# Performance work log

Hardware: AMD Instinct MI355X
Metric: run time of the kernel (lower is better)

The kernel has to match this reference:

```python
import jax, jax.numpy as jnp
import numpy as np

B = 1024       # batch_size b (features has 2*b rows)
DIM = 128      # feature dim
EPS = 1.0      # euclidean eps (module default)


def _make_neighbor_indices(b):
    # negative_samples (2048) >= 2*b - 1 -> deterministic full-batch branch
    idx = np.arange(b)
    not_self = ~np.eye(b, dtype=bool)
    neg1 = np.broadcast_to(idx[None, :], (b, b))[not_self].reshape(b, b - 1)
    neg2 = neg1 + b  # arange(b, 2b) excluding self position
    pos = (idx + b)[:, None]  # positive pair index, column 0
    return np.concatenate([pos, neg1, neg2], axis=1)  # [b, 2b-1]


def setup_inputs() -> dict:
    key = jax.random.key(0)
    features = jax.random.normal(key, (2 * B, DIM), dtype=jnp.float32)
    neigh_inds = jnp.asarray(_make_neighbor_indices(B), dtype=jnp.int64)
    return {"features": features, "neigh_inds": neigh_inds}


def reference(features, neigh_inds):
    b = features.shape[0] // 2
    neighbors = features[neigh_inds]            # [b, 2b-1, d] gather
    origs = features[:b]                        # [b, d]
    # squared euclidean distances anchor -> each neighbor
    dists = jnp.sum((origs[:, None, :] - neighbors) ** 2, axis=2)  # [b, 2b-1]
    probits = 1.0 / (EPS + dists)               # Cauchy kernel
    # infonce: positive is column 0 (clamp is (-inf, inf) -> identity)
    loss = -(jnp.log(probits[:, 0]) - jnp.log(jnp.sum(probits, axis=1)))
    return jnp.mean(loss)
```

## Files before the change

### kernel.cpp

```cpp
#include <hip/hip_runtime.h>
#include <hip/hip_bf16.h>

static constexpr int kB   = 1024;
static constexpr int kNF  = 2048;
static constexpr int kDIM = 128;

typedef __attribute__((ext_vector_type(8))) short  short8;
typedef __attribute__((ext_vector_type(4))) float  floatx4;

__global__ __launch_bounds__(256) void k_prep(const float* __restrict__ F,
                                              __hip_bfloat162* __restrict__ Fb2,
                                              float* __restrict__ norms,
                                              float* __restrict__ S,
                                              float* __restrict__ out) {
    const int t    = threadIdx.x;
    const int lane = t & 63;
    const int row  = blockIdx.x * 4 + (t >> 6);

    const float2 v = *(const float2*)(F + row * kDIM + lane * 2);

    __hip_bfloat162 bv;
    bv.x = __float2bfloat16(v.x);
    bv.y = __float2bfloat16(v.y);
    Fb2[row * (kDIM / 2) + lane] = bv;

    float n = v.x * v.x + v.y * v.y;
    #pragma unroll
    for (int off = 1; off < 64; off <<= 1) n += __shfl_xor(n, off, 64);
    if (lane == 0) norms[row] = n;

    if (blockIdx.x < 4) S[blockIdx.x * 256 + t] = 0.0f;
    if (blockIdx.x == 4 && t == 0) out[0] = 0.0f;
}

static constexpr int kLdsRow = kDIM + 8;

__global__ __launch_bounds__(256) void k_main(const unsigned short* __restrict__ Fb,
                                              const float* __restrict__ norms,
                                              float* __restrict__ S,
                                              float* __restrict__ P) {
    __shared__ unsigned short As[64 * kLdsRow];
    __shared__ unsigned short Bs[64 * kLdsRow];

    const int t  = threadIdx.x;
    const int i0 = blockIdx.x * 64;
    const int k0 = blockIdx.y * 64;

    #pragma unroll
    for (int e = 0; e < 4; ++e) {
        const int idx = e * 256 + t;
        const int row = idx >> 4;
        const int c   = idx & 15;
        const uint4 va = *(const uint4*)(Fb + (i0 + row) * kDIM + c * 8);
        const uint4 vb = *(const uint4*)(Fb + (k0 + row) * kDIM + c * 8);
        *(uint4*)(As + row * kLdsRow + c * 8) = va;
        *(uint4*)(Bs + row * kLdsRow + c * 8) = vb;
    }
    __syncthreads();

    const int lane = t & 63;
    const int w    = t >> 6;
    const int q    = lane >> 4;
    const int c    = lane & 15;

    floatx4 acc[4] = {{0.f,0.f,0.f,0.f},{0.f,0.f,0.f,0.f},
                      {0.f,0.f,0.f,0.f},{0.f,0.f,0.f,0.f}};

    const int arow = w * 16 + c;
    #pragma unroll
    for (int ks = 0; ks < 4; ++ks) {
        const short8 a = *(const short8*)(As + arow * kLdsRow + ks * 32 + q * 8);
        #pragma unroll
        for (int nt = 0; nt < 4; ++nt) {
            const short8 b = *(const short8*)(Bs + (nt * 16 + c) * kLdsRow + ks * 32 + q * 8);
            acc[nt] = __builtin_amdgcn_mfma_f32_16x16x32_bf16(a, b, acc[nt], 0, 0, 0);
        }
    }

    const int ibase = i0 + w * 16 + q * 4;
    float ni[4];
    #pragma unroll
    for (int r = 0; r < 4; ++r) ni[r] = norms[ibase + r];

    float psum[4] = {0.f, 0.f, 0.f, 0.f};
    #pragma unroll
    for (int nt = 0; nt < 4; ++nt) {
        const int   kg = k0 + nt * 16 + c;
        const float nk = norms[kg];
        #pragma unroll
        for (int r = 0; r < 4; ++r) {
            const int ig = ibase + r;
            float dist = ni[r] + nk - 2.0f * acc[nt][r];
            float p    = 1.0f / (1.0f + dist);
            if (kg == ig) p = 0.0f;
            psum[r] += p;
            if (kg == ig + kB) P[ig] = p;
        }
    }

    #pragma unroll
    for (int off = 1; off < 16; off <<= 1) {
        #pragma unroll
        for (int r = 0; r < 4; ++r) psum[r] += __shfl_xor(psum[r], off, 64);
    }
    if (c == 0) {
        #pragma unroll
        for (int r = 0; r < 4; ++r) atomicAdd(&S[ibase + r], psum[r]);
    }
}

__global__ __launch_bounds__(256) void k_final(const float* __restrict__ S,
                                               const float* __restrict__ P,
                                               float* __restrict__ out) {
    const int i = blockIdx.x * 256 + threadIdx.x;
    float l = __logf(S[i]) - __logf(P[i]);
    #pragma unroll
    for (int off = 1; off < 64; off <<= 1) l += __shfl_xor(l, off, 64);
    if ((threadIdx.x & 63) == 0) atomicAdd(out, l * (1.0f / (float)kB));
}

extern "C" void kernel_launch(void* const* d_in, const int* in_sizes, int n_in,
                              void* d_out, int out_size, void* d_ws, size_t ws_size,
                              hipStream_t stream) {
    const float* F = (const float*)d_in[0];
    float* out = (float*)d_out;

    char* ws = (char*)d_ws;
    unsigned short* Fb    = (unsigned short*)ws;
    float*          norms = (float*)(ws + 524288);
    float*          S     = (float*)(ws + 524288 + 8192);
    float*          P     = (float*)(ws + 524288 + 8192 + 4096);

    k_prep <<<dim3(512),    dim3(256), 0, stream>>>(F, (__hip_bfloat162*)Fb, norms, S, out);
    k_main <<<dim3(16, 32), dim3(256), 0, stream>>>(Fb, norms, S, P);
    k_final<<<dim3(4),      dim3(256), 0, stream>>>(S, P, out);
}
```

Baseline: 68.10 us.

## Load MFMA operands directly from global and replace atomics with partial-sum reduction

The main kernel drops its LDS staging and barrier. Each wave now loads its bf16 A and B fragments straight from global memory into registers, with 8 waves per block splitting the 64x64 tile into 16x32 sub-tiles. The row-sum atomics are replaced by per-block partial sums written to a buffer. A single 1024-thread final kernel then reduces those partials and writes the mean, so the zero-initialisation in the prep kernel is no longer needed. This removes atomic contention and LDS traffic, at the cost of redundant global and L2 reads and a larger workspace.

```diff
diff --git a/kernel.cpp b/kernel.cpp
--- a/kernel.cpp
+++ b/kernel.cpp
@@ -1,18 +1,18 @@
 #include <hip/hip_runtime.h>
 #include <hip/hip_bf16.h>
 
+
 static constexpr int kB   = 1024;
-static constexpr int kNF  = 2048;
 static constexpr int kDIM = 128;
+static constexpr int kGX  = 16;
+static constexpr int kGY  = 32;
 
 typedef __attribute__((ext_vector_type(8))) short  short8;
 typedef __attribute__((ext_vector_type(4))) float  floatx4;
 
 __global__ __launch_bounds__(256) void k_prep(const float* __restrict__ F,
                                               __hip_bfloat162* __restrict__ Fb2,
-                                              float* __restrict__ norms,
-                                              float* __restrict__ S,
-                                              float* __restrict__ out) {
+                                              float* __restrict__ norms) {
     const int t    = threadIdx.x;
     const int lane = t & 63;
     const int row  = blockIdx.x * 4 + (t >> 6);
@@ -28,64 +28,55 @@
     #pragma unroll
     for (int off = 1; off < 64; off <<= 1) n += __shfl_xor(n, off, 64);
     if (lane == 0) norms[row] = n;
-
-    if (blockIdx.x < 4) S[blockIdx.x * 256 + t] = 0.0f;
-    if (blockIdx.x == 4 && t == 0) out[0] = 0.0f;
 }
 
-static constexpr int kLdsRow = kDIM + 8;
+__global__ __launch_bounds__(512) void k_main(const unsigned short* __restrict__ Fb,
+                                              const float* __restrict__ norms,
+                                              float* __restrict__ Spart,
+                                              float* __restrict__ P) {
+    __shared__ float sred[4][16][2];
 
-__global__ __launch_bounds__(256) void k_main(const unsigned short* __restrict__ Fb,
-                                              const float* __restrict__ norms,
-                                              float* __restrict__ S,
-                                              float* __restrict__ P) {
-    __shared__ unsigned short As[64 * kLdsRow];
-    __shared__ unsigned short Bs[64 * kLdsRow];
-
-    const int t  = threadIdx.x;
-    const int i0 = blockIdx.x * 64;
-    const int k0 = blockIdx.y * 64;
-
-    #pragma unroll
-    for (int e = 0; e < 4; ++e) {
-        const int idx = e * 256 + t;
-        const int row = idx >> 4;
-        const int c   = idx & 15;
-        const uint4 va = *(const uint4*)(Fb + (i0 + row) * kDIM + c * 8);
-        const uint4 vb = *(const uint4*)(Fb + (k0 + row) * kDIM + c * 8);
-        *(uint4*)(As + row * kLdsRow + c * 8) = va;
-        *(uint4*)(Bs + row * kLdsRow + c * 8) = vb;
-    }
-    __syncthreads();
-
+    const int t    = threadIdx.x;
+    const int w    = t >> 6;
+    const int wi   = w >> 1;
+    const int wk   = w & 1;
     const int lane = t & 63;
-    const int w    = t >> 6;
     const int q    = lane >> 4;
     const int c    = lane & 15;
+    const int i0   = blockIdx.x * 64;
+    const int k0   = blockIdx.y * 64;
 
-    floatx4 acc[4] = {{0.f,0.f,0.f,0.f},{0.f,0.f,0.f,0.f},
-                      {0.f,0.f,0.f,0.f},{0.f,0.f,0.f,0.f}};
+    const unsigned short* Arow = Fb + (i0 + wi * 16 + c) * kDIM;
+    short8 a[4];
+    #pragma unroll
+    for (int ks = 0; ks < 4; ++ks)
+        a[ks] = *(const short8*)(Arow + ks * 32 + q * 8);
 
-    const int arow = w * 16 + c;
+    short8 b[2][4];
+    #pragma unroll
+    for (int nt = 0; nt < 2; ++nt) {
+        const unsigned short* Brow = Fb + (k0 + wk * 32 + nt * 16 + c) * kDIM;
+        #pragma unroll
+        for (int ks = 0; ks < 4; ++ks)
+            b[nt][ks] = *(const short8*)(Brow + ks * 32 + q * 8);
+    }
+
+    floatx4 acc[2] = {{0.f,0.f,0.f,0.f},{0.f,0.f,0.f,0.f}};
     #pragma unroll
     for (int ks = 0; ks < 4; ++ks) {
-        const short8 a = *(const short8*)(As + arow * kLdsRow + ks * 32 + q * 8);
-        #pragma unroll
-        for (int nt = 0; nt < 4; ++nt) {
-            const short8 b = *(const short8*)(Bs + (nt * 16 + c) * kLdsRow + ks * 32 + q * 8);
-            acc[nt] = __builtin_amdgcn_mfma_f32_16x16x32_bf16(a, b, acc[nt], 0, 0, 0);
-        }
+        acc[0] = __builtin_amdgcn_mfma_f32_16x16x32_bf16(a[ks], b[0][ks], acc[0], 0, 0, 0);
+        acc[1] = __builtin_amdgcn_mfma_f32_16x16x32_bf16(a[ks], b[1][ks], acc[1], 0, 0, 0);
     }
 
-    const int ibase = i0 + w * 16 + q * 4;
+    const int ibase = i0 + wi * 16 + q * 4;
     float ni[4];
     #pragma unroll
     for (int r = 0; r < 4; ++r) ni[r] = norms[ibase + r];
 
     float psum[4] = {0.f, 0.f, 0.f, 0.f};
     #pragma unroll
-    for (int nt = 0; nt < 4; ++nt) {
-        const int   kg = k0 + nt * 16 + c;
+    for (int nt = 0; nt < 2; ++nt) {
+        const int   kg = k0 + wk * 32 + nt * 16 + c;
         const float nk = norms[kg];
         #pragma unroll
         for (int r = 0; r < 4; ++r) {
@@ -105,18 +96,37 @@
     }
     if (c == 0) {
         #pragma unroll
-        for (int r = 0; r < 4; ++r) atomicAdd(&S[ibase + r], psum[r]);
+        for (int r = 0; r < 4; ++r) sred[wi][q * 4 + r][wk] = psum[r];
+    }
+    __syncthreads();
+
+    if (t < 64) {
+        const float s = sred[t >> 4][t & 15][0] + sred[t >> 4][t & 15][1];
+        Spart[blockIdx.y * kB + i0 + t] = s;
     }
 }
 
-__global__ __launch_bounds__(256) void k_final(const float* __restrict__ S,
-                                               const float* __restrict__ P,
-                                               float* __restrict__ out) {
-    const int i = blockIdx.x * 256 + threadIdx.x;
-    float l = __logf(S[i]) - __logf(P[i]);
+__global__ __launch_bounds__(1024) void k_final(const float* __restrict__ Spart,
+                                                const float* __restrict__ P,
+                                                float* __restrict__ out) {
+    __shared__ float wred[16];
+    const int t = threadIdx.x;
+
+    float s = 0.f;
+    #pragma unroll
+    for (int kb = 0; kb < kGY; ++kb) s += Spart[kb * kB + t];
+
+    float l = __logf(s) - __logf(P[t]);
     #pragma unroll
     for (int off = 1; off < 64; off <<= 1) l += __shfl_xor(l, off, 64);
-    if ((threadIdx.x & 63) == 0) atomicAdd(out, l * (1.0f / (float)kB));
+    if ((t & 63) == 0) wred[t >> 6] = l;
+    __syncthreads();
+    if (t == 0) {
+        float tot = 0.f;
+        #pragma unroll
+        for (int j = 0; j < 16; ++j) tot += wred[j];
+        out[0] = tot * (1.0f / (float)kB);
+    }
 }
 
 extern "C" void kernel_launch(void* const* d_in, const int* in_sizes, int n_in,
@@ -128,10 +138,10 @@
     char* ws = (char*)d_ws;
     unsigned short* Fb    = (unsigned short*)ws;
     float*          norms = (float*)(ws + 524288);
-    float*          S     = (float*)(ws + 524288 + 8192);
-    float*          P     = (float*)(ws + 524288 + 8192 + 4096);
+    float*          Spart = (float*)(ws + 524288 + 8192);
+    float*          P     = (float*)(ws + 524288 + 8192 + 131072);
 
-    k_prep <<<dim3(512),    dim3(256), 0, stream>>>(F, (__hip_bfloat162*)Fb, norms, S, out);
-    k_main <<<dim3(16, 32), dim3(256), 0, stream>>>(Fb, norms, S, P);
-    k_final<<<dim3(4),      dim3(256), 0, stream>>>(S, P, out);
+    k_prep <<<dim3(512),      dim3(256),  0, stream>>>(F, (__hip_bfloat162*)Fb, norms);
+    k_main <<<dim3(kGX, kGY), dim3(512),  0, stream>>>(Fb, norms, Spart, P);
+    k_final<<<dim3(1),        dim3(1024), 0, stream>>>(Spart, P, out);
 }
```

After: 70.52 us. 1.04x slower.

## Fuse distance GEMM and loss reduction into one kernel, drop the final launch

Applied to the files above, without the earlier changes.

Merges the tiled MFMA distance kernel and the log/mean kernel into one kernel. Each block owns 16 anchor rows and its 8 waves sweep all 2048 columns, reading B fragments straight from global memory instead of staging them in LDS. Row sums are reduced in LDS rather than through global atomics, which removes one launch and the S/P workspace traffic. The trade-off is a grid of only 64 blocks, fewer than the CU count, and uncoalesced direct global fragment loads, so latency hiding may suffer.

```diff
diff --git a/kernel.cpp b/kernel.cpp
--- a/kernel.cpp
+++ b/kernel.cpp
@@ -1,8 +1,8 @@
 #include <hip/hip_runtime.h>
 #include <hip/hip_bf16.h>
 
+
 static constexpr int kB   = 1024;
-static constexpr int kNF  = 2048;
 static constexpr int kDIM = 128;
 
 typedef __attribute__((ext_vector_type(8))) short  short8;
@@ -11,7 +11,6 @@
 __global__ __launch_bounds__(256) void k_prep(const float* __restrict__ F,
                                               __hip_bfloat162* __restrict__ Fb2,
                                               float* __restrict__ norms,
-                                              float* __restrict__ S,
                                               float* __restrict__ out) {
     const int t    = threadIdx.x;
     const int lane = t & 63;
@@ -29,72 +28,73 @@
     for (int off = 1; off < 64; off <<= 1) n += __shfl_xor(n, off, 64);
     if (lane == 0) norms[row] = n;
 
-    if (blockIdx.x < 4) S[blockIdx.x * 256 + t] = 0.0f;
-    if (blockIdx.x == 4 && t == 0) out[0] = 0.0f;
+    if (blockIdx.x == 0 && t == 0) out[0] = 0.0f;
 }
 
-static constexpr int kLdsRow = kDIM + 8;
+__global__ __launch_bounds__(512) void k_fused(const unsigned short* __restrict__ Fb,
+                                               const float* __restrict__ norms,
+                                               float* __restrict__ out) {
+    __shared__ float Swave[16][9];
+    __shared__ float Pl[16];
 
-__global__ __launch_bounds__(256) void k_main(const unsigned short* __restrict__ Fb,
-                                              const float* __restrict__ norms,
-                                              float* __restrict__ S,
-                                              float* __restrict__ P) {
-    __shared__ unsigned short As[64 * kLdsRow];
-    __shared__ unsigned short Bs[64 * kLdsRow];
-
-    const int t  = threadIdx.x;
-    const int i0 = blockIdx.x * 64;
-    const int k0 = blockIdx.y * 64;
-
-    #pragma unroll
-    for (int e = 0; e < 4; ++e) {
-        const int idx = e * 256 + t;
-        const int row = idx >> 4;
-        const int c   = idx & 15;
-        const uint4 va = *(const uint4*)(Fb + (i0 + row) * kDIM + c * 8);
-        const uint4 vb = *(const uint4*)(Fb + (k0 + row) * kDIM + c * 8);
-        *(uint4*)(As + row * kLdsRow + c * 8) = va;
-        *(uint4*)(Bs + row * kLdsRow + c * 8) = vb;
-    }
-    __syncthreads();
-
+    const int t    = threadIdx.x;
+    const int w    = t >> 6;
     const int lane = t & 63;
-    const int w    = t >> 6;
     const int q    = lane >> 4;
     const int c    = lane & 15;
+    const int i0   = blockIdx.x * 16;
 
-    floatx4 acc[4] = {{0.f,0.f,0.f,0.f},{0.f,0.f,0.f,0.f},
-                      {0.f,0.f,0.f,0.f},{0.f,0.f,0.f,0.f}};
+    const unsigned short* Arow = Fb + (i0 + c) * kDIM;
+    short8 a[4];
+    #pragma unroll
+    for (int ks = 0; ks < 4; ++ks)
+        a[ks] = *(const short8*)(Arow + ks * 32 + q * 8);
 
-    const int arow = w * 16 + c;
-    #pragma unroll
-    for (int ks = 0; ks < 4; ++ks) {
-        const short8 a = *(const short8*)(As + arow * kLdsRow + ks * 32 + q * 8);
-        #pragma unroll
-        for (int nt = 0; nt < 4; ++nt) {
-            const short8 b = *(const short8*)(Bs + (nt * 16 + c) * kLdsRow + ks * 32 + q * 8);
-            acc[nt] = __builtin_amdgcn_mfma_f32_16x16x32_bf16(a, b, acc[nt], 0, 0, 0);
-        }
-    }
-
-    const int ibase = i0 + w * 16 + q * 4;
+    const int i0q = i0 + q * 4;
     float ni[4];
     #pragma unroll
-    for (int r = 0; r < 4; ++r) ni[r] = norms[ibase + r];
+    for (int r = 0; r < 4; ++r) ni[r] = norms[i0q + r];
 
     float psum[4] = {0.f, 0.f, 0.f, 0.f};
-    #pragma unroll
-    for (int nt = 0; nt < 4; ++nt) {
-        const int   kg = k0 + nt * 16 + c;
-        const float nk = norms[kg];
+    const int kbase = w * 256;
+
+    #pragma unroll 2
+    for (int kt = 0; kt < 16; kt += 2) {
+        const int k0a = kbase + kt * 16;
+        const int k0b = k0a + 16;
+        const unsigned short* Ba = Fb + (k0a + c) * kDIM;
+        const unsigned short* Bb = Fb + (k0b + c) * kDIM;
+        short8 ba[4], bb[4];
+        #pragma unroll
+        for (int ks = 0; ks < 4; ++ks) {
+            ba[ks] = *(const short8*)(Ba + ks * 32 + q * 8);
+            bb[ks] = *(const short8*)(Bb + ks * 32 + q * 8);
+        }
+        floatx4 acc0 = {0.f,0.f,0.f,0.f};
+        floatx4 acc1 = {0.f,0.f,0.f,0.f};
+        #pragma unroll
+        for (int ks = 0; ks < 4; ++ks) {
+            acc0 = __builtin_amdgcn_mfma_f32_16x16x32_bf16(a[ks], ba[ks], acc0, 0, 0, 0);
+            acc1 = __builtin_amdgcn_mfma_f32_16x16x32_bf16(a[ks], bb[ks], acc1, 0, 0, 0);
+        }
+        const float nka = norms[k0a + c];
+        const float nkb = norms[k0b + c];
+        const int   kga = k0a + c;
+        const int   kgb = k0b + c;
         #pragma unroll
         for (int r = 0; r < 4; ++r) {
-            const int ig = ibase + r;
-            float dist = ni[r] + nk - 2.0f * acc[nt][r];
-            float p    = 1.0f / (1.0f + dist);
-            if (kg == ig) p = 0.0f;
-            psum[r] += p;
-            if (kg == ig + kB) P[ig] = p;
+            const int ig = i0q + r;
+            float da = ni[r] + nka - 2.0f * acc0[r];
+            float pa = 1.0f / (1.0f + da);
+            if (kga == ig) pa = 0.0f;
+            psum[r] += pa;
+            if (kga == ig + kB) Pl[q * 4 + r] = pa;
+
+            float db = ni[r] + nkb - 2.0f * acc1[r];
+            float pb = 1.0f / (1.0f + db);
+            if (kgb == ig) pb = 0.0f;
+            psum[r] += pb;
+            if (kgb == ig + kB) Pl[q * 4 + r] = pb;
         }
     }
 
@@ -105,18 +105,19 @@
     }
     if (c == 0) {
         #pragma unroll
-        for (int r = 0; r < 4; ++r) atomicAdd(&S[ibase + r], psum[r]);
+        for (int r = 0; r < 4; ++r) Swave[q * 4 + r][w] = psum[r];
     }
-}
+    __syncthreads();
 
-__global__ __launch_bounds__(256) void k_final(const float* __restrict__ S,
-                                               const float* __restrict__ P,
-                                               float* __restrict__ out) {
-    const int i = blockIdx.x * 256 + threadIdx.x;
-    float l = __logf(S[i]) - __logf(P[i]);
-    #pragma unroll
-    for (int off = 1; off < 64; off <<= 1) l += __shfl_xor(l, off, 64);
-    if ((threadIdx.x & 63) == 0) atomicAdd(out, l * (1.0f / (float)kB));
+    if (t < 16) {
+        float S = 0.f;
+        #pragma unroll
+        for (int w8 = 0; w8 < 8; ++w8) S += Swave[t][w8];
+        float l = __logf(S) - __logf(Pl[t]);
+        #pragma unroll
+        for (int off = 1; off < 16; off <<= 1) l += __shfl_xor(l, off, 64);
+        if (t == 0) atomicAdd(out, l * (1.0f / (float)kB));
+    }
 }
 
 extern "C" void kernel_launch(void* const* d_in, const int* in_sizes, int n_in,
@@ -128,10 +129,7 @@
     char* ws = (char*)d_ws;
     unsigned short* Fb    = (unsigned short*)ws;
     float*          norms = (float*)(ws + 524288);
-    float*          S     = (float*)(ws + 524288 + 8192);
-    float*          P     = (float*)(ws + 524288 + 8192 + 4096);
 
-    k_prep <<<dim3(512),    dim3(256), 0, stream>>>(F, (__hip_bfloat162*)Fb, norms, S, out);
-    k_main <<<dim3(16, 32), dim3(256), 0, stream>>>(Fb, norms, S, P);
-    k_final<<<dim3(4),      dim3(256), 0, stream>>>(S, P, out);
+    k_prep <<<dim3(512), dim3(256), 0, stream>>>(F, (__hip_bfloat162*)Fb, norms, out);
+    k_fused<<<dim3(64),  dim3(512), 0, stream>>>(Fb, norms, out);
 }
```

Result: slower. 80.22 us (+17.8%).
